# Kernel tuning notes

Hardware: AMD Instinct MI355X
Metric: run time of the kernel (lower is better)

## Reference

```python
import jax, jax.numpy as jnp
import numpy as np

N = 50000
E = 800000
H = 64
IN_NF = 8
EA = 2
N_LAYERS = 4
INNER = 7.0        # module.n_layers set to 7 when varDT=False (integration step count)
COORDS_WEIGHT = 1.0
EPS = 1e-8


def _mlp2(x, W1, b1, W2, b2, act_last=False):
    h = jax.nn.silu(x @ W1 + b1)
    h = h @ W2 + b2
    return jax.nn.silu(h) if act_last else h


def setup_inputs() -> dict:
    key = jax.random.key(0)
    ks = jax.random.split(key, 20)
    def g(k, shape, scale=None):
        s = scale if scale is not None else 1.0 / np.sqrt(shape[0])
        return (jax.random.normal(k, shape, jnp.float32) * s).astype(jnp.float32)
    return {
        "his": jax.random.normal(ks[0], (N, IN_NF), jnp.float32),
        "loc": jax.random.normal(ks[1], (N, 3), jnp.float32),
        "edges": jax.random.randint(ks[2], (2, E), 0, N),
        "vel": jax.random.normal(ks[3], (N, 3), jnp.float32),
        "edge_attr": jax.random.normal(ks[4], (E, EA), jnp.float32),
        "emb_W": g(ks[5], (IN_NF, H)), "emb_b": jnp.zeros((H,), jnp.float32),
        "e_W1": g(ks[6], (2 * H + 1 + EA, H)), "e_b1": jnp.zeros((H,), jnp.float32),
        "e_W2": g(ks[7], (H, H)), "e_b2": jnp.zeros((H,), jnp.float32),
        "c_W1": g(ks[8], (H, H)), "c_b1": jnp.zeros((H,), jnp.float32),
        "c_W2": g(ks[9], (H, 1), scale=1e-3),  # last coord layer: no bias, small init
        "v_W1": g(ks[10], (H, H)), "v_b1": jnp.zeros((H,), jnp.float32),
        "v_W2": g(ks[11], (H, 1)), "v_b2": jnp.zeros((1,), jnp.float32),
        "n_W1": g(ks[12], (2 * H, H)), "n_b1": jnp.zeros((H,), jnp.float32),
        "n_W2": g(ks[13], (H, H)), "n_b2": jnp.zeros((H,), jnp.float32),
    }


def _egcl(h, coord, vel, init_vel, row, col, edge_attr, p):
    # edge model: gather -> MLP
    coord_diff = coord[row] - coord[col]                         # [E,3]
    radial = jnp.sum(coord_diff * coord_diff, -1, keepdims=True)  # [E,1]
    e_in = jnp.concatenate([h[row], h[col], radial, edge_attr], -1)
    m = _mlp2(e_in, p["e_W1"], p["e_b1"], p["e_W2"], p["e_b2"], act_last=True)  # [E,H]
    # equivariant coordinate message + scatter-mean aggregation
    w = jax.nn.silu(m @ p["c_W1"] + p["c_b1"]) @ p["c_W2"]      # [E,1]
    trans = coord_diff * w                                       # [E,3]
    num = jax.ops.segment_sum(trans, row, num_segments=h.shape[0])
    cnt = jax.ops.segment_sum(jnp.ones((row.shape[0], 1), coord.dtype), row, num_segments=h.shape[0])
    acc = COORDS_WEIGHT * num / jnp.maximum(cnt, 1.0)            # [N,3]
    # second-order (velocity) update with learned gate + speed renorm (norm_vel=True)
    v_scale = _mlp2(h, p["v_W1"], p["v_b1"], p["v_W2"], p["v_b2"])  # [N,1]
    vel = v_scale * vel + acc / INNER
    speed0 = jnp.linalg.norm(init_vel, axis=-1, keepdims=True)
    vel = vel / (jnp.linalg.norm(vel, axis=-1, keepdims=True) + EPS) * speed0
    coord = coord + vel / INNER
    # node model: scatter-sum edge features + residual MLP (recurrent=True)
    agg_h = jax.ops.segment_sum(m, row, num_segments=h.shape[0])
    h_out = h + _mlp2(jnp.concatenate([h, agg_h], -1), p["n_W1"], p["n_b1"], p["n_W2"], p["n_b2"])
    return h_out, coord, vel


def reference(his, loc, edges, vel, edge_attr, emb_W, emb_b, e_W1, e_b1, e_W2, e_b2,
              c_W1, c_b1, c_W2, v_W1, v_b1, v_W2, v_b2, n_W1, n_b1, n_W2, n_b2):
    p = dict(e_W1=e_W1, e_b1=e_b1, e_W2=e_W2, e_b2=e_b2, c_W1=c_W1, c_b1=c_b1, c_W2=c_W2,
             v_W1=v_W1, v_b1=v_b1, v_W2=v_W2, v_b2=v_b2, n_W1=n_W1, n_b1=n_b1, n_W2=n_W2, n_b2=n_b2)
    row, col = edges[0], edges[1]
    his_e = his @ emb_W + emb_b                                  # embedding
    h1, x, v = _egcl(his_e, loc, vel, vel, row, col, edge_attr, p)
    h = his_e + h1
    for _ in range(1, N_LAYERS):                                 # shared-weight recurrent module
        hi, x, v = _egcl(h, x, v, vel, row, col, edge_attr, p)
        h = h + hi
    return (x, h, v)
```

## Files before the change

kernel.cpp:

```cpp
#include <hip/hip_runtime.h>
#include <hip/hip_bf16.h>
#include <stdint.h>

#define NN 50000
#define EE 800000
#define HD 64
#define AGS 72
#define SCL 1.4426950408889634f
#define LN2 0.6931471805599453f

typedef short short8 __attribute__((ext_vector_type(8)));
typedef float f32x4  __attribute__((ext_vector_type(4)));
typedef float f32x16 __attribute__((ext_vector_type(16)));
typedef uint  uint2v __attribute__((ext_vector_type(2)));

__device__ __forceinline__ float b2f(ushort u){ return __uint_as_float(((uint32_t)u)<<16); }
__device__ __forceinline__ ushort f2b(float f){
  uint32_t u = __float_as_uint(f);
  u += 0x7fffu + ((u>>16)&1u);
  return (ushort)(u>>16);
}
__device__ __forceinline__ uint pk2(float lo, float hi){
  union { __hip_bfloat162 b; uint u; } x;
  x.b = __float22bfloat162_rn(make_float2(lo, hi));
  return x.u;
}
__device__ __forceinline__ float silu_f(float x){
  return x * __builtin_amdgcn_rcpf(1.0f + __expf(-x));
}
__device__ __forceinline__ float exp2_fast(float x){
#if __has_builtin(__builtin_amdgcn_exp2f)
  return __builtin_amdgcn_exp2f(x);
#else
  float r; asm("v_exp_f32 %0, %1" : "=v"(r) : "v"(x)); return r;
#endif
}
__device__ __forceinline__ float silu_s(float xs){
  return xs * __builtin_amdgcn_rcpf(1.0f + exp2_fast(-xs));
}

__global__ __launch_bounds__(256) void k_prep(
    const int* __restrict__ erow, int* __restrict__ counts,
    const float* __restrict__ loc, const float* __restrict__ vel0,
    float4* __restrict__ coordw4, float4* __restrict__ velw4,
    const float* __restrict__ his, const float* __restrict__ embW,
    const float* __restrict__ embB, float* __restrict__ h, ushort* __restrict__ hb,
    const float* __restrict__ eW1, const float* __restrict__ eB1,
    const float* __restrict__ eW2, const float* __restrict__ eB2,
    const float* __restrict__ cW1, const float* __restrict__ cB1,
    const float* __restrict__ nW1, const float* __restrict__ nW2,
    const float* __restrict__ vW1, ushort* __restrict__ allp)
{
  int gid = blockIdx.x*256 + threadIdx.x;
  if (gid < NN*HD){
    int n = gid >> 6, j = gid & 63;
    float s = embB[j];
    #pragma unroll
    for (int k = 0; k < 8; ++k) s += his[n*8 + k] * embW[k*64 + j];
    h[gid] = s;
    hb[gid] = f2b(s);
  }
  if (gid < EE) atomicAdd(&counts[erow[gid]], 1);
  if (gid < NN){
    float vx = vel0[gid*3+0], vy = vel0[gid*3+1], vz = vel0[gid*3+2];
    float sp = sqrtf(vx*vx + vy*vy + vz*vz);
    velw4[gid] = make_float4(vx, vy, vz, sp);
    coordw4[gid] = make_float4(loc[gid*3+0], loc[gid*3+1], loc[gid*3+2], 0.0f);
  }
  if (gid < 35840){
    int idx = gid;
    float v;
    if (idx < 19456){
      int rel; const float* src; const float* bias; int mode;
      if (idx < 9216){ rel = idx; src = eW1; bias = eB1; mode = 0; }
      else if (idx < 14336){ rel = idx - 9216; src = eW2; bias = eB2; mode = 1; }
      else { rel = idx - 14336; src = cW1; bias = cB1; mode = 2; }
      int u = rel >> 9;
      int kt = u >> 1, mt = u & 1;
      int within = rel & 511;
      int lane = within >> 3, i = within & 7;
      int col = mt*32 + (lane & 31);
      if (mode == 0){
        int k = kt*16 + (lane>>5)*8 + i;
        if (k < 131) v = src[k*64 + col] * SCL;
        else if (k == 131) v = bias[col] * SCL;
        else v = 0.0f;
      } else if (mode == 1){
        int k = kt*16 + (lane>>5)*8 + i;
        if (k < 64) v = src[k*64 + col];
        else if (k == 64) v = bias[col] * SCL;
        else v = 0.0f;
      } else {
        if (kt < 4){
          int k = 32*(kt>>1) + 16*(kt&1) + 8*(i>>2) + 2*((i>>1)&1) + (i&1) + 4*(lane>>5);
          v = src[k*64 + col];
        } else {
          int k = 64 + (lane>>5)*8 + i;
          v = (k == 64) ? bias[col] * SCL : 0.0f;
        }
      }
    } else {
      int rel = idx - 19456;
      const float* src; int kt; int Ksrc; int isN1 = 0;
      if (rel < 8192){ src = nW1; kt = rel >> 11; Ksrc = 128; isN1 = 1; }
      else if (rel < 12288){ src = nW2; kt = (rel - 8192) >> 11; Ksrc = 64; }
      else { src = vW1; kt = (rel - 12288) >> 11; Ksrc = 64; }
      int within = rel & 2047;
      int i = within & 7;
      int lane = (within >> 3) & 63;
      int ct = (within >> 9) & 3;
      int k = kt*32 + (lane>>4)*8 + i;
      int col = ct*16 + (lane & 15);
      v = (k < Ksrc) ? src[k*64 + col] : 0.0f;
      if (isN1 && k >= 64) v *= LN2;
    }
    allp[idx] = f2b(v);
  }
}

__global__ __launch_bounds__(256) void k_bsum(const int* __restrict__ counts, int* __restrict__ bsum){
  __shared__ int sm[4];
  int tid = threadIdx.x;
  int i = blockIdx.x*256 + tid;
  int v = (i < NN) ? counts[i] : 0;
  #pragma unroll
  for (int off = 1; off < 64; off <<= 1) v += __shfl_xor(v, off);
  if ((tid & 63) == 0) sm[tid >> 6] = v;
  __syncthreads();
  if (tid == 0) bsum[blockIdx.x] = sm[0] + sm[1] + sm[2] + sm[3];
}

__global__ __launch_bounds__(256) void k_bscan(const int* __restrict__ bsum, int* __restrict__ bbase){
  __shared__ int sm[256];
  int tid = threadIdx.x;
  int v = (tid < 196) ? bsum[tid] : 0;
  sm[tid] = v;
  __syncthreads();
  #pragma unroll
  for (int off = 1; off < 256; off <<= 1){
    int t = (tid >= off) ? sm[tid - off] : 0;
    __syncthreads();
    sm[tid] += t;
    __syncthreads();
  }
  if (tid < 196) bbase[tid] = sm[tid] - v;
}

__global__ __launch_bounds__(256) void k_scatter(const int* __restrict__ counts,
    const int* __restrict__ bbase, int* __restrict__ cursor){
  __shared__ int sm[256];
  int tid = threadIdx.x;
  int i = blockIdx.x*256 + tid;
  int v = (i < NN) ? counts[i] : 0;
  sm[tid] = v;
  __syncthreads();
  #pragma unroll
  for (int off = 1; off < 256; off <<= 1){
    int t = (tid >= off) ? sm[tid - off] : 0;
    __syncthreads();
    sm[tid] += t;
    __syncthreads();
  }
  if (i < NN) cursor[i] = bbase[blockIdx.x] + sm[tid] - v;
}

__global__ __launch_bounds__(256) void k_fill(const int* __restrict__ erow,
    const int* __restrict__ ecol, const float* __restrict__ eattr,
    int* __restrict__ cursor, int4* __restrict__ erec){
  int e = blockIdx.x*256 + threadIdx.x;
  if (e < EE){
    int r = erow[e];
    int pos = atomicAdd(&cursor[r], 1);
    int4 rec;
    rec.x = r;
    rec.y = ecol[e];
    rec.z = __float_as_int(eattr[(size_t)e*2 + 0]);
    rec.w = __float_as_int(eattr[(size_t)e*2 + 1]);
    erec[pos] = rec;
  }
}

__global__ __launch_bounds__(64, 4) void k_edge(
    const ushort* __restrict__ hb, const float4* __restrict__ coord4,
    const int4* __restrict__ erec,
    const ushort* __restrict__ W1p, const ushort* __restrict__ W2p, const ushort* __restrict__ C1p,
    const float* __restrict__ cw2,
    float* __restrict__ aggf)
{
  __shared__ __align__(16) uint XMT[32*38];
  const int lane = threadIdx.x & 63;
  const int e = lane & 31, h = lane >> 5;

  const int bid = blockIdx.x;
  const int swz = (bid & 7)*3125 + (bid >> 3);
  const int slot = swz*32 + e;

  int4 er = erec[slot];
  const int rA = er.x, cA = er.y;

  float4 crd = coord4[rA], ccd = coord4[cA];
  float dx = crd.x-ccd.x, dy = crd.y-ccd.y, dz = crd.z-ccd.z;
  float radial = dx*dx + dy*dy + dz*dz;

  const short8* W1f = reinterpret_cast<const short8*>(W1p);
  const short8* W2f = reinterpret_cast<const short8*>(W2p);
  const short8* C1f = reinterpret_cast<const short8*>(C1p);
  const int wrow = e*38;

  short8 ones8 = {0,0,0,0,0,0,0,0};
  if (h == 0) ones8[0] = (short)0x3F80;

  {
    short8 bf[9];
    #pragma unroll
    for (int kt = 0; kt < 4; ++kt)
      bf[kt] = *reinterpret_cast<const short8*>(hb + (size_t)rA*HD + kt*16 + h*8);
    #pragma unroll
    for (int kt = 0; kt < 4; ++kt)
      bf[4+kt] = *reinterpret_cast<const short8*>(hb + (size_t)cA*HD + kt*16 + h*8);
    short8 t8 = {0,0,0,0,0,0,0,0};
    if (h == 0){
      t8[0] = (short)f2b(radial);
      t8[1] = (short)f2b(__int_as_float(er.z));
      t8[2] = (short)f2b(__int_as_float(er.w));
      t8[3] = (short)0x3F80;
    }
    bf[8] = t8;

    f32x16 a0, a1;
    #pragma unroll
    for (int r = 0; r < 16; ++r){ a0[r] = 0.0f; a1[r] = 0.0f; }
    __builtin_amdgcn_s_setprio(1);
    #pragma unroll
    for (int kt = 0; kt < 9; ++kt)
      a0 = __builtin_amdgcn_mfma_f32_32x32x16_bf16(W1f[(kt*2+0)*64 + lane], bf[kt], a0, 0,0,0);
    #pragma unroll
    for (int kt = 0; kt < 9; ++kt)
      a1 = __builtin_amdgcn_mfma_f32_32x32x16_bf16(W1f[(kt*2+1)*64 + lane], bf[kt], a1, 0,0,0);
    __builtin_amdgcn_s_setprio(0);
    #pragma unroll
    for (int q = 0; q < 4; ++q){
      uint u0 = pk2(silu_s(a0[4*q+0]), silu_s(a0[4*q+1]));
      uint u1 = pk2(silu_s(a0[4*q+2]), silu_s(a0[4*q+3]));
      *reinterpret_cast<uint2v*>(&XMT[wrow + q*4 + h*2]) = (uint2v){u0, u1};
    }
    #pragma unroll
    for (int q = 0; q < 4; ++q){
      uint u0 = pk2(silu_s(a1[4*q+0]), silu_s(a1[4*q+1]));
      uint u1 = pk2(silu_s(a1[4*q+2]), silu_s(a1[4*q+3]));
      *reinterpret_cast<uint2v*>(&XMT[wrow + 16 + q*4 + h*2]) = (uint2v){u0, u1};
    }
  }
  __builtin_amdgcn_sched_barrier(0);

  uint uw2[16];
  {
    short8 xf[4];
    #pragma unroll
    for (int kt = 0; kt < 4; ++kt)
      xf[kt] = *reinterpret_cast<const short8*>(&XMT[wrow + kt*8 + h*4]);
    f32x16 a0, a1;
    #pragma unroll
    for (int r = 0; r < 16; ++r){ a0[r] = 0.0f; a1[r] = 0.0f; }
    __builtin_amdgcn_s_setprio(1);
    #pragma unroll
    for (int kt = 0; kt < 4; ++kt)
      a0 = __builtin_amdgcn_mfma_f32_32x32x16_bf16(W2f[(kt*2+0)*64 + lane], xf[kt], a0, 0,0,0);
    a0 = __builtin_amdgcn_mfma_f32_32x32x16_bf16(W2f[(4*2+0)*64 + lane], ones8, a0, 0,0,0);
    #pragma unroll
    for (int kt = 0; kt < 4; ++kt)
      a1 = __builtin_amdgcn_mfma_f32_32x32x16_bf16(W2f[(kt*2+1)*64 + lane], xf[kt], a1, 0,0,0);
    a1 = __builtin_amdgcn_mfma_f32_32x32x16_bf16(W2f[(4*2+1)*64 + lane], ones8, a1, 0,0,0);
    __builtin_amdgcn_s_setprio(0);
    #pragma unroll
    for (int s = 0; s < 8; ++s) uw2[s]   = pk2(silu_s(a0[2*s]), silu_s(a0[2*s+1]));
    #pragma unroll
    for (int s = 0; s < 8; ++s) uw2[8+s] = pk2(silu_s(a1[2*s]), silu_s(a1[2*s+1]));
    #pragma unroll
    for (int t = 0; t < 8; ++t)
      *reinterpret_cast<uint2v*>(&XMT[wrow + h*16 + 2*t]) = (uint2v){uw2[2*t], uw2[2*t+1]};
  }

  float pw = 0.0f;
  {
    union U4 { uint u[4]; short8 s; };
    f32x16 a0, a1;
    #pragma unroll
    for (int r = 0; r < 16; ++r){ a0[r] = 0.0f; a1[r] = 0.0f; }
    __builtin_amdgcn_s_setprio(1);
    #pragma unroll
    for (int kt = 0; kt < 4; ++kt){
      U4 t; t.u[0]=uw2[4*kt+0]; t.u[1]=uw2[4*kt+1]; t.u[2]=uw2[4*kt+2]; t.u[3]=uw2[4*kt+3];
      a0 = __builtin_amdgcn_mfma_f32_32x32x16_bf16(C1f[(kt*2+0)*64 + lane], t.s, a0, 0,0,0);
    }
    a0 = __builtin_amdgcn_mfma_f32_32x32x16_bf16(C1f[(4*2+0)*64 + lane], ones8, a0, 0,0,0);
    #pragma unroll
    for (int kt = 0; kt < 4; ++kt){
      U4 t; t.u[0]=uw2[4*kt+0]; t.u[1]=uw2[4*kt+1]; t.u[2]=uw2[4*kt+2]; t.u[3]=uw2[4*kt+3];
      a1 = __builtin_amdgcn_mfma_f32_32x32x16_bf16(C1f[(kt*2+1)*64 + lane], t.s, a1, 0,0,0);
    }
    a1 = __builtin_amdgcn_mfma_f32_32x32x16_bf16(C1f[(4*2+1)*64 + lane], ones8, a1, 0,0,0);
    __builtin_amdgcn_s_setprio(0);
    #pragma unroll
    for (int q = 0; q < 4; ++q){
      f32x4 cwq = *reinterpret_cast<const f32x4*>(cw2 + q*8 + h*4);
      #pragma unroll
      for (int r = 0; r < 4; ++r) pw += silu_s(a0[4*q+r]) * cwq[r];
    }
    #pragma unroll
    for (int q = 0; q < 4; ++q){
      f32x4 cwq = *reinterpret_cast<const f32x4*>(cw2 + 32 + q*8 + h*4);
      #pragma unroll
      for (int r = 0; r < 4; ++r) pw += silu_s(a1[4*q+r]) * cwq[r];
    }
  }
  pw += __shfl_xor(pw, 32);
  pw *= LN2;
  if (h == 0){
    *reinterpret_cast<uint2v*>(&XMT[wrow + 32]) =
        (uint2v){__float_as_uint(dx*pw), __float_as_uint(dy*pw)};
    XMT[wrow + 34] = __float_as_uint(dz*pw);
  }
  __builtin_amdgcn_sched_barrier(0);

  const int j = lane;
  const int soff = (((j>>5)*8 + ((j>>3)&3)*2 + ((j>>1)&1)) + ((j>>2)&1)*16)*2 + (j&1);
  const ushort* mvals = reinterpret_cast<const ushort*>(XMT);
  const float*  tvals = reinterpret_cast<const float*>(XMT);
  float sum = 0.f, ts = 0.f;
  int rcur = __builtin_amdgcn_readlane(rA, 0);
  int segstart = 0;
  #pragma unroll
  for (int i = 0; i < 32; ++i){
    sum += b2f(mvals[i*76 + soff]);
    if (lane < 3) ts += tvals[i*38 + 32 + lane];
    int rnext = (i < 31) ? __builtin_amdgcn_readlane(rA, i+1) : -1;
    if (rnext != rcur){
      if (segstart == 0 || i == 31){
        atomicAdd(&aggf[(size_t)rcur*AGS + lane], sum);
        if (lane < 3) atomicAdd(&aggf[(size_t)rcur*AGS + 64 + lane], ts);
      } else {
        aggf[(size_t)rcur*AGS + lane] = sum;
        if (lane < 3) aggf[(size_t)rcur*AGS + 64 + lane] = ts;
      }
      sum = 0.f; ts = 0.f; rcur = rnext; segstart = i + 1;
    }
  }
}

__global__ __launch_bounds__(256) void k_node(
    const ushort* __restrict__ hb, float* __restrict__ aggf, const float* __restrict__ h_in,
    const ushort* __restrict__ nW1p, const ushort* __restrict__ nW2p, const ushort* __restrict__ vW1p,
    const float* __restrict__ nb1, const float* __restrict__ nb2,
    const float* __restrict__ vb1, const float* __restrict__ vW2, const float* __restrict__ vb2,
    const int* __restrict__ counts, float4* __restrict__ velw4, float4* __restrict__ coordw4,
    float* __restrict__ h_out, ushort* __restrict__ hb_out,
    float* __restrict__ xout, float* __restrict__ vout, int last)
{
  __shared__ __align__(16) ushort HID[64*88];
  __shared__ float VS[64];
  const int tid = threadIdx.x;
  const int wave = tid >> 6, lane = tid & 63;
  const int c = lane & 15, g = lane >> 4;
  const int wt = wave * 16;
  const int nbase = blockIdx.x * 64;
  int nA = nbase + wt + c;
  int nAc = (nA < NN) ? nA : (NN-1);

  short8 af[4];
  af[0] = *reinterpret_cast<const short8*>(hb + (size_t)nAc*HD + g*8);
  af[1] = *reinterpret_cast<const short8*>(hb + (size_t)nAc*HD + 32 + g*8);
  {
    const float* ag = aggf + (size_t)nAc*AGS;
    f32x4 q0 = *reinterpret_cast<const f32x4*>(ag + g*8);
    f32x4 q1 = *reinterpret_cast<const f32x4*>(ag + g*8 + 4);
    f32x4 q2 = *reinterpret_cast<const f32x4*>(ag + 32 + g*8);
    f32x4 q3 = *reinterpret_cast<const f32x4*>(ag + 32 + g*8 + 4);
    union FB { ushort u[8]; short8 s; };
    FB f2_, f3_;
    #pragma unroll
    for (int i = 0; i < 4; ++i){ f2_.u[i] = f2b(q0[i]); f2_.u[4+i] = f2b(q1[i]); }
    #pragma unroll
    for (int i = 0; i < 4; ++i){ f3_.u[i] = f2b(q2[i]); f3_.u[4+i] = f2b(q3[i]); }
    af[2] = f2_.s;
    af[3] = f3_.s;
  }
  const short8* N1f = reinterpret_cast<const short8*>(nW1p);
  const short8* N2f = reinterpret_cast<const short8*>(nW2p);
  const short8* V1f = reinterpret_cast<const short8*>(vW1p);

  f32x4 acc[4];
  #pragma unroll
  for (int ct = 0; ct < 4; ++ct){
    float bb = nb1[ct*16 + c];
    acc[ct] = (f32x4){bb,bb,bb,bb};
  }
  #pragma unroll
  for (int kt = 0; kt < 4; ++kt){
    #pragma unroll
    for (int ct = 0; ct < 4; ++ct){
      acc[ct] = __builtin_amdgcn_mfma_f32_16x16x32_bf16(af[kt], N1f[(kt*4+ct)*64 + lane], acc[ct], 0,0,0);
    }
  }
  #pragma unroll
  for (int ct = 0; ct < 4; ++ct){
    int col = ct*16 + c;
    #pragma unroll
    for (int r = 0; r < 4; ++r){
      HID[(wt + g*4 + r)*88 + col] = f2b(silu_f(acc[ct][r]));
    }
  }

  f32x4 av[4];
  #pragma unroll
  for (int ct = 0; ct < 4; ++ct){
    float bb = vb1[ct*16 + c];
    av[ct] = (f32x4){bb,bb,bb,bb};
  }
  #pragma unroll
  for (int kt = 0; kt < 2; ++kt){
    #pragma unroll
    for (int ct = 0; ct < 4; ++ct){
      av[ct] = __builtin_amdgcn_mfma_f32_16x16x32_bf16(af[kt], V1f[(kt*4+ct)*64 + lane], av[ct], 0,0,0);
    }
  }
  float pw[4] = {0.f,0.f,0.f,0.f};
  #pragma unroll
  for (int ct = 0; ct < 4; ++ct){
    float vw = vW2[ct*16 + c];
    #pragma unroll
    for (int r = 0; r < 4; ++r) pw[r] += silu_f(av[ct][r]) * vw;
  }
  #pragma unroll
  for (int off = 1; off < 16; off <<= 1){
    #pragma unroll
    for (int r = 0; r < 4; ++r) pw[r] += __shfl_xor(pw[r], off, 16);
  }
  if (c == 0){
    float vbias = vb2[0];
    #pragma unroll
    for (int r = 0; r < 4; ++r) VS[wt + g*4 + r] = pw[r] + vbias;
  }

  short8 h0 = *reinterpret_cast<const short8*>(&HID[(wt + c)*88 + g*8]);
  short8 h1 = *reinterpret_cast<const short8*>(&HID[(wt + c)*88 + 32 + g*8]);
  f32x4 a2[4];
  #pragma unroll
  for (int ct = 0; ct < 4; ++ct){
    float bb = nb2[ct*16 + c];
    a2[ct] = (f32x4){bb,bb,bb,bb};
  }
  #pragma unroll
  for (int ct = 0; ct < 4; ++ct)
    a2[ct] = __builtin_amdgcn_mfma_f32_16x16x32_bf16(h0, N2f[(0*4+ct)*64 + lane], a2[ct], 0,0,0);
  #pragma unroll
  for (int ct = 0; ct < 4; ++ct)
    a2[ct] = __builtin_amdgcn_mfma_f32_16x16x32_bf16(h1, N2f[(1*4+ct)*64 + lane], a2[ct], 0,0,0);
  #pragma unroll
  for (int ct = 0; ct < 4; ++ct){
    int col = ct*16 + c;
    #pragma unroll
    for (int r = 0; r < 4; ++r){
      int n = nbase + wt + g*4 + r;
      if (n < NN){
        size_t off = (size_t)n*HD + col;
        float v = 2.0f*h_in[off] + a2[ct][r];
        h_out[off] = v;
        hb_out[off] = f2b(v);
      }
    }
  }

  __syncthreads();
  if (tid < 64){
    int n = nbase + tid;
    if (n < NN){
      float vsn = VS[tid];
      float inv = 1.0f / fmaxf((float)counts[n], 1.0f);
      const float* ag = aggf + (size_t)n*AGS + 64;
      float ax = ag[0]*inv, ay = ag[1]*inv, az = ag[2]*inv;
      float4 vv = velw4[n];
      float4 cc = coordw4[n];
      float v0 = vsn*vv.x + ax*(1.0f/7.0f);
      float v1 = vsn*vv.y + ay*(1.0f/7.0f);
      float v2 = vsn*vv.z + az*(1.0f/7.0f);
      float s = vv.w / (sqrtf(v0*v0 + v1*v1 + v2*v2) + 1e-8f);
      v0 *= s; v1 *= s; v2 *= s;
      float c0 = cc.x + v0*(1.0f/7.0f);
      float c1 = cc.y + v1*(1.0f/7.0f);
      float c2 = cc.z + v2*(1.0f/7.0f);
      if (last){
        vout[n*3+0] = v0; vout[n*3+1] = v1; vout[n*3+2] = v2;
        xout[n*3+0] = c0; xout[n*3+1] = c1; xout[n*3+2] = c2;
      } else {
        velw4[n] = make_float4(v0, v1, v2, vv.w);
        coordw4[n] = make_float4(c0, c1, c2, 0.0f);
      }
    }
  }

  __syncthreads();
  int nvalid = NN - nbase; if (nvalid > 64) nvalid = 64;
  f32x4* zb4 = reinterpret_cast<f32x4*>(aggf + (size_t)nbase*AGS);
  f32x4 z4 = {0.f,0.f,0.f,0.f};
  for (int idx2 = tid; idx2 < nvalid*(AGS/4); idx2 += 256) zb4[idx2] = z4;
}

extern "C" void kernel_launch(void* const* d_in, const int* in_sizes, int n_in,
                              void* d_out, int out_size, void* d_ws, size_t ws_size,
                              hipStream_t stream)
{
  const float* his  = (const float*)d_in[0];
  const float* loc  = (const float*)d_in[1];
  const int*   edges= (const int*)d_in[2];
  const float* vel0 = (const float*)d_in[3];
  const float* eatt = (const float*)d_in[4];
  const float* embW = (const float*)d_in[5];
  const float* embB = (const float*)d_in[6];
  const float* eW1  = (const float*)d_in[7];
  const float* eB1  = (const float*)d_in[8];
  const float* eW2  = (const float*)d_in[9];
  const float* eB2  = (const float*)d_in[10];
  const float* cW1  = (const float*)d_in[11];
  const float* cB1  = (const float*)d_in[12];
  const float* cW2  = (const float*)d_in[13];
  const float* vW1  = (const float*)d_in[14];
  const float* vB1  = (const float*)d_in[15];
  const float* vW2  = (const float*)d_in[16];
  const float* vB2  = (const float*)d_in[17];
  const float* nW1  = (const float*)d_in[18];
  const float* nB1  = (const float*)d_in[19];
  const float* nW2  = (const float*)d_in[20];
  const float* nB2  = (const float*)d_in[21];
  const int* erow = edges;
  const int* ecol = edges + EE;

  char* ws = (char*)d_ws;
  size_t off = 0;
  auto alloc = [&](size_t bytes)->char*{
    char* p = ws + off;
    off = (off + bytes + 255) & ~(size_t)255;
    return p;
  };
  ushort* hb     = (ushort*)alloc((size_t)NN*HD*2);
  int*    counts = (int*)   alloc((size_t)NN*4);
  float*  aggf   = (float*) alloc((size_t)NN*AGS*4);
  int*    cursor = (int*)   alloc((size_t)NN*4);
  int*    bsum   = (int*)   alloc(256*4);
  int*    bbase  = (int*)   alloc(256*4);
  float4* coordw4= (float4*)alloc((size_t)NN*16);
  float4* velw4  = (float4*)alloc((size_t)NN*16);
  ushort* allp   = (ushort*)alloc(35840*2);
  int4*   erec   = (int4*)  alloc((size_t)EE*16);

  ushort* eW1p32 = allp;
  ushort* eW2p32 = allp + 9216;
  ushort* cW1p32 = allp + 14336;
  ushort* nW1p   = allp + 19456;
  ushort* nW2p   = allp + 27648;
  ushort* vW1p   = allp + 31744;

  float* xout = (float*)d_out;
  float* hout = (float*)d_out + (size_t)NN*3;
  float* vout = (float*)d_out + (size_t)NN*3 + (size_t)NN*HD;

  size_t counts_pad = ((size_t)NN*4 + 255) & ~(size_t)255;
  hipMemsetAsync(counts, 0, counts_pad + (size_t)NN*AGS*4, stream);
  k_prep<<<12500,256,0,stream>>>(erow, counts, loc, vel0, coordw4, velw4,
      his, embW, embB, hout, hb,
      eW1, eB1, eW2, eB2, cW1, cB1, nW1, nW2, vW1, allp);
  k_bsum<<<196,256,0,stream>>>(counts, bsum);
  k_bscan<<<1,256,0,stream>>>(bsum, bbase);
  k_scatter<<<196,256,0,stream>>>(counts, bbase, cursor);
  k_fill<<<3125,256,0,stream>>>(erow, ecol, eatt, cursor, erec);

  for (int L = 0; L < 4; ++L){
    k_edge<<<25000,64,0,stream>>>(hb, coordw4, erec,
        eW1p32, eW2p32, cW1p32, cW2, aggf);
    k_node<<<782,256,0,stream>>>(hb, aggf, hout, nW1p, nW2p, vW1p,
        nB1, nB2, vB1, vW2, vB2, counts, velw4, coordw4,
        hout, hb, xout, vout, (L==3) ? 1 : 0);
  }
}
```

Measured before the change: 456.1 us.

## Keep first-layer edge MLP output in registers and pack two waves per block

The first edge-MLP layer's activations are now passed straight into the second layer's MFMAs from registers instead of going through a shared-memory round trip. To make this work, the packing of the eW2 weights is switched to the same permuted K-order already used for cW1. The edge kernel also now runs two waves of 32 edges each per 128-thread block, with a revised XCD swizzle and a higher occupancy hint. This removes LDS writes and reads and a scheduling barrier, but the larger block doubles LDS per block and the launch-bounds change may alter register allocation.

```diff
diff --git a/kernel.cpp b/kernel.cpp
--- a/kernel.cpp
+++ b/kernel.cpp
@@ -73,7 +73,7 @@
     if (idx < 19456){
       int rel; const float* src; const float* bias; int mode;
       if (idx < 9216){ rel = idx; src = eW1; bias = eB1; mode = 0; }
-      else if (idx < 14336){ rel = idx - 9216; src = eW2; bias = eB2; mode = 1; }
+      else if (idx < 14336){ rel = idx - 9216; src = eW2; bias = eB2; mode = 2; }
       else { rel = idx - 14336; src = cW1; bias = cB1; mode = 2; }
       int u = rel >> 9;
       int kt = u >> 1, mt = u & 1;
@@ -84,11 +84,6 @@
         int k = kt*16 + (lane>>5)*8 + i;
         if (k < 131) v = src[k*64 + col] * SCL;
         else if (k == 131) v = bias[col] * SCL;
-        else v = 0.0f;
-      } else if (mode == 1){
-        int k = kt*16 + (lane>>5)*8 + i;
-        if (k < 64) v = src[k*64 + col];
-        else if (k == 64) v = bias[col] * SCL;
         else v = 0.0f;
       } else {
         if (kt < 4){
@@ -180,20 +175,23 @@
   }
 }
 
-__global__ __launch_bounds__(64, 4) void k_edge(
+__global__ __launch_bounds__(128, 5) void k_edge(
     const ushort* __restrict__ hb, const float4* __restrict__ coord4,
     const int4* __restrict__ erec,
     const ushort* __restrict__ W1p, const ushort* __restrict__ W2p, const ushort* __restrict__ C1p,
     const float* __restrict__ cw2,
     float* __restrict__ aggf)
 {
-  __shared__ __align__(16) uint XMT[32*38];
-  const int lane = threadIdx.x & 63;
+  __shared__ __align__(16) uint XMT[64*38];
+  const int tid = threadIdx.x;
+  const int wave = tid >> 6, lane = tid & 63;
   const int e = lane & 31, h = lane >> 5;
+  const int wt = wave * 32;
 
   const int bid = blockIdx.x;
-  const int swz = (bid & 7)*3125 + (bid >> 3);
-  const int slot = swz*32 + e;
+  const int xcd = bid & 7, bx = bid >> 3;
+  const int swz = (xcd < 4) ? (xcd*1563 + bx) : (4*1563 + (xcd-4)*1562 + bx);
+  const int slot = swz*64 + wt + e;
 
   int4 er = erec[slot];
   const int rA = er.x, cA = er.y;
@@ -205,11 +203,14 @@
   const short8* W1f = reinterpret_cast<const short8*>(W1p);
   const short8* W2f = reinterpret_cast<const short8*>(W2p);
   const short8* C1f = reinterpret_cast<const short8*>(C1p);
-  const int wrow = e*38;
+  const int wrow = (wt + e)*38;
 
   short8 ones8 = {0,0,0,0,0,0,0,0};
   if (h == 0) ones8[0] = (short)0x3F80;
 
+  union U4 { uint u[4]; short8 s; };
+
+  uint uw[16];
   {
     short8 bf[9];
     #pragma unroll
@@ -239,37 +240,28 @@
       a1 = __builtin_amdgcn_mfma_f32_32x32x16_bf16(W1f[(kt*2+1)*64 + lane], bf[kt], a1, 0,0,0);
     __builtin_amdgcn_s_setprio(0);
     #pragma unroll
-    for (int q = 0; q < 4; ++q){
-      uint u0 = pk2(silu_s(a0[4*q+0]), silu_s(a0[4*q+1]));
-      uint u1 = pk2(silu_s(a0[4*q+2]), silu_s(a0[4*q+3]));
-      *reinterpret_cast<uint2v*>(&XMT[wrow + q*4 + h*2]) = (uint2v){u0, u1};
-    }
-    #pragma unroll
-    for (int q = 0; q < 4; ++q){
-      uint u0 = pk2(silu_s(a1[4*q+0]), silu_s(a1[4*q+1]));
-      uint u1 = pk2(silu_s(a1[4*q+2]), silu_s(a1[4*q+3]));
-      *reinterpret_cast<uint2v*>(&XMT[wrow + 16 + q*4 + h*2]) = (uint2v){u0, u1};
-    }
-  }
-  __builtin_amdgcn_sched_barrier(0);
+    for (int s = 0; s < 8; ++s) uw[s]   = pk2(silu_s(a0[2*s]), silu_s(a0[2*s+1]));
+    #pragma unroll
+    for (int s = 0; s < 8; ++s) uw[8+s] = pk2(silu_s(a1[2*s]), silu_s(a1[2*s+1]));
+  }
 
   uint uw2[16];
   {
-    short8 xf[4];
-    #pragma unroll
-    for (int kt = 0; kt < 4; ++kt)
-      xf[kt] = *reinterpret_cast<const short8*>(&XMT[wrow + kt*8 + h*4]);
     f32x16 a0, a1;
     #pragma unroll
     for (int r = 0; r < 16; ++r){ a0[r] = 0.0f; a1[r] = 0.0f; }
     __builtin_amdgcn_s_setprio(1);
     #pragma unroll
-    for (int kt = 0; kt < 4; ++kt)
-      a0 = __builtin_amdgcn_mfma_f32_32x32x16_bf16(W2f[(kt*2+0)*64 + lane], xf[kt], a0, 0,0,0);
+    for (int kt = 0; kt < 4; ++kt){
+      U4 t; t.u[0]=uw[4*kt+0]; t.u[1]=uw[4*kt+1]; t.u[2]=uw[4*kt+2]; t.u[3]=uw[4*kt+3];
+      a0 = __builtin_amdgcn_mfma_f32_32x32x16_bf16(W2f[(kt*2+0)*64 + lane], t.s, a0, 0,0,0);
+    }
     a0 = __builtin_amdgcn_mfma_f32_32x32x16_bf16(W2f[(4*2+0)*64 + lane], ones8, a0, 0,0,0);
     #pragma unroll
-    for (int kt = 0; kt < 4; ++kt)
-      a1 = __builtin_amdgcn_mfma_f32_32x32x16_bf16(W2f[(kt*2+1)*64 + lane], xf[kt], a1, 0,0,0);
+    for (int kt = 0; kt < 4; ++kt){
+      U4 t; t.u[0]=uw[4*kt+0]; t.u[1]=uw[4*kt+1]; t.u[2]=uw[4*kt+2]; t.u[3]=uw[4*kt+3];
+      a1 = __builtin_amdgcn_mfma_f32_32x32x16_bf16(W2f[(kt*2+1)*64 + lane], t.s, a1, 0,0,0);
+    }
     a1 = __builtin_amdgcn_mfma_f32_32x32x16_bf16(W2f[(4*2+1)*64 + lane], ones8, a1, 0,0,0);
     __builtin_amdgcn_s_setprio(0);
     #pragma unroll
@@ -283,7 +275,6 @@
 
   float pw = 0.0f;
   {
-    union U4 { uint u[4]; short8 s; };
     f32x16 a0, a1;
     #pragma unroll
     for (int r = 0; r < 16; ++r){ a0[r] = 0.0f; a1[r] = 0.0f; }
@@ -332,8 +323,8 @@
   int segstart = 0;
   #pragma unroll
   for (int i = 0; i < 32; ++i){
-    sum += b2f(mvals[i*76 + soff]);
-    if (lane < 3) ts += tvals[i*38 + 32 + lane];
+    sum += b2f(mvals[(wt + i)*76 + soff]);
+    if (lane < 3) ts += tvals[(wt + i)*38 + 32 + lane];
     int rnext = (i < 31) ? __builtin_amdgcn_readlane(rA, i+1) : -1;
     if (rnext != rcur){
       if (segstart == 0 || i == 31){
@@ -575,7 +566,7 @@
   k_fill<<<3125,256,0,stream>>>(erow, ecol, eatt, cursor, erec);
 
   for (int L = 0; L < 4; ++L){
-    k_edge<<<25000,64,0,stream>>>(hb, coordw4, erec,
+    k_edge<<<12500,128,0,stream>>>(hb, coordw4, erec,
         eW1p32, eW2p32, cW1p32, cW2, aggf);
     k_node<<<782,256,0,stream>>>(hb, aggf, hout, nW1p, nW2p, vW1p,
         nB1, nB2, vB1, vW2, vB2, counts, velw4, coordw4,
```

Result: slower. 573.9 us (+25.8%).
